# Kernel tuning notes

Measured on AMD Instinct MI355X. Metric: run time of the kernel, lower is better.

Reference implementation:

```python
import jax, jax.numpy as jnp
import numpy as np

B, T = 4096, 35          # batch rallies, max_ball_round
DSE = 227                # state_embed_dim = (37-2) + 64 + 64 + 64
C = 64                   # context_dim
H = 1024                 # hidden_dim
G5 = 25                  # GMM_num * 5
S = 12                   # shot_num
SE_NOCTX = DSE - C       # 163, state_embedding features before prior_z concat


def setup_inputs() -> dict:
    key = jax.random.key(0)
    ks = jax.random.split(key, 24)
    def r(i, shape, s=0.05):
        return (jax.random.normal(ks[i], shape, jnp.float32) * s)
    return {
        "state_embedding": r(0, (B, T, SE_NOCTX), 1.0),
        "prior_z": r(1, (B, C), 1.0),
        # state_ref_encoder (no bias)
        "W_ref": r(2, (T * DSE, DSE), 0.01),
        # f_decoder: DSE -> H -> H -> DSE with Softplus
        "fW1": r(3, (DSE, H)), "fb1": jnp.zeros((H,), jnp.float32),
        "fW2": r(4, (H, H)),   "fb2": jnp.zeros((H,), jnp.float32),
        "fW3": r(5, (H, DSE)), "fb3": jnp.zeros((DSE,), jnp.float32),
        # g_nets: DSE independent Linear(1,DSE)->Softplus->Linear(DSE,1)->Sigmoid, stacked
        "gW1": r(6, (DSE, DSE), 0.01), "gb1": r(7, (DSE, DSE), 0.01),
        "gW2": r(8, (DSE, DSE), 0.01), "gb2": r(9, (DSE,), 0.01),
        # GMM / shot heads on f_latent (no bias)
        "W_land": r(10, (DSE, G5), 0.01),
        "W_shot": r(11, (DSE, S), 0.01),
        "W_move": r(12, (DSE, G5), 0.01),
        # context_decoder: C -> H -> H -> C with Softplus
        "cW1": r(13, (C, H)), "cb1": jnp.zeros((H,), jnp.float32),
        "cW2": r(14, (H, H)), "cb2": jnp.zeros((H,), jnp.float32),
        "cW3": r(15, (H, C)), "cb3": jnp.zeros((C,), jnp.float32),
        # context GMM / shot heads (no bias)
        "cW_land": r(16, (C, G5), 0.01),
        "cW_shot": r(17, (C, S), 0.01),
        "cW_move": r(18, (C, G5), 0.01),
    }


def reference(state_embedding, prior_z, W_ref,
              fW1, fb1, fW2, fb2, fW3, fb3,
              gW1, gb1, gW2, gb2,
              W_land, W_shot, W_move,
              cW1, cb1, cW2, cb2, cW3, cb3,
              cW_land, cW_shot, cW_move):
    sp = jax.nn.softplus
    b, t, _ = state_embedding.shape

    # context_decoder(prior_z)
    ch = sp(prior_z @ cW1 + cb1)
    ch = sp(ch @ cW2 + cb2)
    ctx = ch @ cW3 + cb3                                  # [B, C]

    # repeat prior_z along time, concat, flatten, state_ref_encoder
    prior_rep = jnp.broadcast_to(prior_z[:, None, :], (b, t, prior_z.shape[-1]))
    sre = jnp.concatenate([state_embedding, prior_rep], axis=-1)  # [B, T, DSE]
    f_input = sre.reshape(b, -1) @ W_ref                  # [B, DSE]

    # f_decoder
    fh = sp(f_input @ fW1 + fb1)
    fh = sp(fh @ fW2 + fb2)
    f_latent = fh @ fW3 + fb3                             # [B, DSE]

    # g(): DSE per-dim tiny MLPs, fully vectorized as batched einsum
    gh = sp(f_latent[:, :, None] * gW1[None, :, :] + gb1[None, :, :])  # [B, DSE, DSE]
    g_out = jax.nn.sigmoid(jnp.einsum('bdh,dh->bd', gh, gW2) + gb2)    # [B, DSE]

    # GMM / shot heads
    land = f_latent @ W_land                              # [B, 25]
    shot = jax.nn.log_softmax(f_latent @ W_shot, axis=-1) # [B, 12]
    move = f_latent @ W_move                              # [B, 25]
    c_land = ctx @ cW_land
    c_shot = jax.nn.log_softmax(ctx @ cW_shot, axis=-1)
    c_move = ctx @ cW_move

    return jnp.concatenate([land, shot, move, g_out, c_land, c_shot, c_move, ctx], axis=-1)  # [B, 415]
```

## Files before the change

### kernel.cpp

```cpp
#include <hip/hip_runtime.h>
#include <hip/hip_bf16.h>

using s8 = __attribute__((ext_vector_type(8))) short;
using f4 = __attribute__((ext_vector_type(4))) float;
using us8 = __attribute__((ext_vector_type(8))) unsigned short;

__device__ __forceinline__ void glds16(const void* g, void* l) {
    __builtin_amdgcn_global_load_lds(
        (const __attribute__((address_space(1))) void*)g,
        (__attribute__((address_space(3))) void*)l, 16, 0, 0);
}

__device__ __forceinline__ unsigned short f2b(float f) {
    union { float f; unsigned u; } v; v.f = f;
    unsigned r = v.u + 0x7fffu + ((v.u >> 16) & 1u);
    return (unsigned short)(r >> 16);
}
__device__ __forceinline__ float softplus_f(float x) {
    return fmaxf(x, 0.f) + __logf(1.f + __expf(-fabsf(x)));
}
__device__ __forceinline__ float sigmoid_f(float x) {
    return 1.f / (1.f + __expf(-x));
}
__device__ __forceinline__ float exp2_f(float x) {
    float r; asm("v_exp_f32 %0, %1" : "=v"(r) : "v"(x)); return r;
}
__device__ __forceinline__ float log2_f(float x) {
    float r; asm("v_log_f32 %0, %1" : "=v"(r) : "v"(x)); return r;
}

__device__ __forceinline__ float lse12(const float* s) {
    float m = s[0];
#pragma unroll
    for (int j = 1; j < 12; j++) m = fmaxf(m, s[j]);
    float sum = 0.f;
#pragma unroll
    for (int j = 0; j < 12; j++) sum += __expf(s[j] - m);
    return m + __logf(sum);
}

__global__ __launch_bounds__(256) void prep_all_k(
    const float* __restrict__ cW1, const float* __restrict__ cW2,
    const float* __restrict__ cW3, const float* __restrict__ fW1,
    const float* __restrict__ fW2, const float* __restrict__ fW3,
    unsigned short* __restrict__ cW1T, unsigned short* __restrict__ cW2T,
    unsigned short* __restrict__ cW3T, unsigned short* __restrict__ fW1T,
    unsigned short* __restrict__ fW2T, unsigned short* __restrict__ fW3T,
    const float* __restrict__ Wref, unsigned short* __restrict__ WcatT,
    const float* __restrict__ pz, unsigned short* __restrict__ pzb,
    const float* __restrict__ gb1, const float* __restrict__ gW2,
    float* __restrict__ b1s, float* __restrict__ w2s,
    const float* __restrict__ Wl, const float* __restrict__ Ws,
    const float* __restrict__ Wm, const float* __restrict__ cWl,
    const float* __restrict__ cWs, const float* __restrict__ cWm,
    unsigned short* __restrict__ WhcT,
    const float* __restrict__ se, unsigned short* __restrict__ Acat) {
    __shared__ float tile[32][33];
    const int b = blockIdx.x, t = threadIdx.x;
    if (b < 2752) {
        int z, r = b;
        if (r < 64) { z = 0; }
        else if (r < 1088) { z = 1; r -= 64; }
        else if (r < 1216) { z = 2; r -= 1088; }
        else if (r < 1472) { z = 3; r -= 1216; }
        else if (r < 2496) { z = 4; r -= 1472; }
        else { z = 5; r -= 2496; }
        const float* src = z == 0 ? cW1 : z == 1 ? cW2 : z == 2 ? cW3
                          : z == 3 ? fW1 : z == 4 ? fW2 : fW3;
        unsigned short* dst = z == 0 ? cW1T : z == 1 ? cW2T : z == 2 ? cW3T
                             : z == 3 ? fW1T : z == 4 ? fW2T : fW3T;
        const int K    = z == 0 ? 64 : z == 3 ? 227 : 1024;
        const int N    = z == 2 ? 64 : z == 5 ? 227 : 1024;
        const int Kpad = z == 0 ? 64 : z == 3 ? 256 : 1024;
        const int Npad = z == 2 ? 128 : z == 5 ? 256 : 1024;
        const int nbx = Npad >> 5;
        const int bx = r % nbx, by = r / nbx;
        const int n0 = bx * 32, k0 = by * 32;
        const int tx = t & 31, ty = t >> 5;
#pragma unroll
        for (int rr = 0; rr < 4; rr++) {
            int k = k0 + ty + rr * 8, n = n0 + tx;
            tile[ty + rr * 8][tx] = (k < K && n < N) ? src[(size_t)k * N + n] : 0.f;
        }
        __syncthreads();
#pragma unroll
        for (int rr = 0; rr < 4; rr++) {
            int n = n0 + ty + rr * 8, k = k0 + tx;
            dst[(size_t)n * Kpad + k] = f2b(tile[tx][ty + rr * 8]);
        }
    } else if (b < 4200) {
        const int r = b - 2752;
        const int n0 = (r & 7) * 32, k0 = (r >> 3) * 32;
        const int tx = t & 31, ty = t >> 5;
#pragma unroll
        for (int rr = 0; rr < 4; rr++) {
            int k = k0 + ty + rr * 8, n = n0 + tx;
            float v = 0.f;
            if (n < 227 && k < 5769) {
                if (k < 5705) {
                    int wrow = k + 64 * (k / 163);
                    v = Wref[(size_t)wrow * 227 + n];
                } else {
                    int j2 = k - 5705;
                    for (int tt = 0; tt < 35; tt++)
                        v += Wref[(size_t)(tt * 227 + 163 + j2) * 227 + n];
                }
            }
            tile[ty + rr * 8][tx] = v;
        }
        __syncthreads();
#pragma unroll
        for (int rr = 0; rr < 4; rr++) {
            int n = n0 + ty + rr * 8, k = k0 + tx;
            if (n < 256 && k < 5792) dst_write: ;
            if (n < 256 && k < 5792)
                WcatT[(size_t)n * 5792 + k] = f2b(tile[tx][ty + rr * 8]);
        }
    } else if (b < 5586) {
        constexpr int NCVT = 4096 * 64;
        constexpr int NGS = 227 * 227;
        constexpr int NW = 128 * 320;
        int i = (b - 4200) * 256 + t;
        if (i < NCVT) {
            pzb[i] = f2b(pz[i]);
        } else if (i < NCVT + NGS) {
            int j = i - NCVT;
            b1s[j] = gb1[j] * 1.44269504f;
            w2s[j] = gW2[j] * 0.69314718f;
        } else if (i < NCVT + NGS + NW) {
            int j = i - NCVT - NGS;
            int n = j / 320, k = j - n * 320;
            float v = 0.f;
            if (n < 62 && k < 227) {
                if (n < 25)      v = Wl[(size_t)k * 25 + n];
                else if (n < 37) v = Ws[(size_t)k * 12 + (n - 25)];
                else             v = Wm[(size_t)k * 25 + (n - 37)];
            } else if (n >= 64 && n < 126 && k >= 256) {
                const int jj = n - 64, kk = k - 256;
                if (jj < 25)      v = cWl[(size_t)kk * 25 + jj];
                else if (jj < 37) v = cWs[(size_t)kk * 12 + (jj - 25)];
                else              v = cWm[(size_t)kk * 25 + (jj - 37)];
            }
            WhcT[(size_t)n * 320 + k] = f2b(v);
        }
    } else {
        const int r = b - 5586;
        const int c = (r % 3) * 256 + t;
        const int row = r / 3;
        if (c >= 724) return;
        const int col0 = c * 8;
        us8 o;
        if (col0 + 8 <= 5705) {
            const float* s = se + (size_t)row * 5705 + col0;
#pragma unroll
            for (int j = 0; j < 8; j++) o[j] = f2b(s[j]);
        } else {
#pragma unroll
            for (int j = 0; j < 8; j++) {
                int col = col0 + j;
                float v = 0.f;
                if (col < 5705) v = se[(size_t)row * 5705 + col];
                else if (col < 5769) v = pz[(size_t)row * 64 + (col - 5705)];
                o[j] = f2b(v);
            }
        }
        *(us8*)(Acat + (size_t)row * 5792 + col0) = o;
    }
}

__global__ __launch_bounds__(256) void red_enc4(const float* __restrict__ part,
                                                unsigned short* __restrict__ finb) {
    const int t = threadIdx.x;
    const int row = blockIdx.y * 4 + (t >> 6);
    const int cw = t & 63;
    if (cw < 57) {
        const float* p = part + (size_t)row * 228 + cw * 4;
        float4 s = make_float4(0.f, 0.f, 0.f, 0.f);
#pragma unroll
        for (int z = 0; z < 6; z++) {
            float4 v = *(const float4*)(p + (size_t)z * 4096 * 228);
            s.x += v.x; s.y += v.y; s.z += v.z; s.w += v.w;
        }
        if (cw == 56) s.w = 0.f;
        ushort4 o;
        o.x = f2b(s.x); o.y = f2b(s.y); o.z = f2b(s.z); o.w = f2b(s.w);
        *(ushort4*)(finb + (size_t)row * 256 + cw * 4) = o;
    } else {
        ushort4 z4 = make_ushort4(0, 0, 0, 0);
        *(ushort4*)(finb + (size_t)row * 256 + 228 + (cw - 57) * 4) = z4;
    }
}

__global__ __launch_bounds__(256) void red_cf3_k(
    const float* __restrict__ part_c3, const float* __restrict__ cb3,
    float* __restrict__ ctxb,
    const float* __restrict__ part_f3, const float* __restrict__ fb3,
    float* __restrict__ flat) {
    const int bx = blockIdx.x, t = threadIdx.x;
    if (bx < 256) {
        int idx = bx * 256 + t;
        int row = idx >> 4, c4 = idx & 15;
        float4 s = *(const float4*)(cb3 + c4 * 4);
        const float* p = part_c3 + (size_t)row * 64 + c4 * 4;
#pragma unroll
        for (int z = 0; z < 8; z++) {
            float4 v = *(const float4*)(p + (size_t)z * 4096 * 64);
            s.x += v.x; s.y += v.y; s.z += v.z; s.w += v.w;
        }
        *(float4*)(ctxb + (size_t)row * 64 + c4 * 4) = s;
    } else {
        const int by = bx - 256;
        const int row = by * 4 + (t >> 6);
        const int cw = t & 63;
        if (cw >= 57) return;
        float b[4];
#pragma unroll
        for (int j = 0; j < 4; j++) {
            int col = cw * 4 + j;
            b[j] = (col < 227) ? fb3[col] : 0.f;
        }
        const float* p = part_f3 + (size_t)row * 228 + cw * 4;
        float4 s = make_float4(b[0], b[1], b[2], b[3]);
#pragma unroll
        for (int z = 0; z < 4; z++) {
            float4 v = *(const float4*)(p + (size_t)z * 4096 * 228);
            s.x += v.x; s.y += v.y; s.z += v.z; s.w += v.w;
        }
        if (cw == 56) s.w = 0.f;
        *(float4*)(flat + (size_t)row * 228 + cw * 4) = s;
    }
}

template <int CM, int ACT, bool OBF16>
__global__ __launch_bounds__(256) void gemm_dma(
    const unsigned short* __restrict__ A, int lda,
    const unsigned short* __restrict__ WT, int ldwt,
    const float* __restrict__ bias,
    void* __restrict__ Cptr, int ldc, int N, int K, int kchunk) {
    __shared__ __align__(16) unsigned short As[128 * 32];
    __shared__ __align__(16) unsigned short Bs[128 * 32];
    const int tid = threadIdx.x;
    const int m0 = blockIdx.y * 128, n0 = blockIdx.x * 128;
    const int kbeg = blockIdx.z * kchunk;
    const int kend = min(kbeg + kchunk, K);
    const int lane = tid & 63, w = tid >> 6;
    const int wm = w >> 1, wn = w & 1;
    const int quad = lane >> 4, l16 = lane & 15;
    const int dr = lane >> 2;
    const int dk = (lane & 3) * 8;

    f4 acc[4][4] = {};

    for (int k0 = kbeg; k0 < kend; k0 += 32) {
#pragma unroll
        for (int c = 0; c < 2; c++) {
            int rr = w * 32 + c * 16;
            glds16(A + (size_t)(m0 + rr + dr) * lda + k0 + dk, &As[rr * 32]);
            glds16(WT + (size_t)(n0 + rr + dr) * ldwt + k0 + dk, &Bs[rr * 32]);
        }
        __syncthreads();
        s8 a[4], b[4];
#pragma unroll
        for (int mi = 0; mi < 4; mi++)
            a[mi] = *(const s8*)&As[(wm * 64 + mi * 16 + l16) * 32 + quad * 8];
#pragma unroll
        for (int ni = 0; ni < 4; ni++)
            b[ni] = *(const s8*)&Bs[(wn * 64 + ni * 16 + l16) * 32 + quad * 8];
#pragma unroll
        for (int mi = 0; mi < 4; mi++)
#pragma unroll
            for (int ni = 0; ni < 4; ni++)
                acc[mi][ni] = __builtin_amdgcn_mfma_f32_16x16x32_bf16(
                    a[mi], b[ni], acc[mi][ni], 0, 0, 0);
        __syncthreads();
    }

    const size_t zoff = (CM == 2) ? (size_t)blockIdx.z * 4096 * ldc : 0;
#pragma unroll
    for (int mi = 0; mi < 4; mi++) {
        int gmb = m0 + wm * 64 + mi * 16 + quad * 4;
#pragma unroll
        for (int ni = 0; ni < 4; ni++) {
            int gn = n0 + wn * 64 + ni * 16 + l16;
            if (gn < N) {
#pragma unroll
                for (int r = 0; r < 4; r++) {
                    float v = acc[mi][ni][r];
                    size_t off = (size_t)(gmb + r) * ldc + gn;
                    if (CM == 2) {
                        ((float*)Cptr)[zoff + off] = v;
                    } else {
                        if (bias) v += bias[gn];
                        if (ACT == 1) v = softplus_f(v);
                        if (OBF16) ((unsigned short*)Cptr)[off] = f2b(v);
                        else ((float*)Cptr)[off] = v;
                    }
                }
            }
        }
    }
}

__global__ __launch_bounds__(256) void gemm_dualg(
    const unsigned short* __restrict__ A0, int lda0, int K0,
    const unsigned short* __restrict__ A1, int lda1, int K1,
    const unsigned short* __restrict__ W0, int ldw0,
    const unsigned short* __restrict__ W1, int ldw1,
    const float* __restrict__ b0, const float* __restrict__ b1,
    unsigned short* __restrict__ C0, unsigned short* __restrict__ C1) {
    __shared__ __align__(16) unsigned short As[128 * 32];
    __shared__ __align__(16) unsigned short Bs[128 * 32];
    const int z = blockIdx.z;
    const unsigned short* __restrict__ A  = z ? A1 : A0;
    const unsigned short* __restrict__ WT = z ? W1 : W0;
    const float* __restrict__ bias        = z ? b1 : b0;
    unsigned short* __restrict__ C        = z ? C1 : C0;
    const int lda = z ? lda1 : lda0;
    const int ldw = z ? ldw1 : ldw0;
    const int K   = z ? K1 : K0;
    const int tid = threadIdx.x;
    const int m0 = blockIdx.y * 128, n0 = blockIdx.x * 128;
    const int lane = tid & 63, w = tid >> 6;
    const int wm = w >> 1, wn = w & 1;
    const int quad = lane >> 4, l16 = lane & 15;
    const int dr = lane >> 2;
    const int dk = (lane & 3) * 8;

    f4 acc[4][4] = {};

    for (int k0 = 0; k0 < K; k0 += 32) {
#pragma unroll
        for (int c = 0; c < 2; c++) {
            int rr = w * 32 + c * 16;
            glds16(A + (size_t)(m0 + rr + dr) * lda + k0 + dk, &As[rr * 32]);
            glds16(WT + (size_t)(n0 + rr + dr) * ldw + k0 + dk, &Bs[rr * 32]);
        }
        __syncthreads();
        s8 a[4], b[4];
#pragma unroll
        for (int mi = 0; mi < 4; mi++)
            a[mi] = *(const s8*)&As[(wm * 64 + mi * 16 + l16) * 32 + quad * 8];
#pragma unroll
        for (int ni = 0; ni < 4; ni++)
            b[ni] = *(const s8*)&Bs[(wn * 64 + ni * 16 + l16) * 32 + quad * 8];
#pragma unroll
        for (int mi = 0; mi < 4; mi++)
#pragma unroll
            for (int ni = 0; ni < 4; ni++)
                acc[mi][ni] = __builtin_amdgcn_mfma_f32_16x16x32_bf16(
                    a[mi], b[ni], acc[mi][ni], 0, 0, 0);
        __syncthreads();
    }

#pragma unroll
    for (int mi = 0; mi < 4; mi++) {
        int gmb = m0 + wm * 64 + mi * 16 + quad * 4;
#pragma unroll
        for (int ni = 0; ni < 4; ni++) {
            int gn = n0 + wn * 64 + ni * 16 + l16;
#pragma unroll
            for (int r = 0; r < 4; r++) {
                float v = acc[mi][ni][r] + bias[gn];
                C[(size_t)(gmb + r) * 1024 + gn] = f2b(softplus_f(v));
            }
        }
    }
}

__global__ __launch_bounds__(256) void part_cf3_k(
    const unsigned short* __restrict__ h2c, const unsigned short* __restrict__ cW3T,
    const unsigned short* __restrict__ h2f, const unsigned short* __restrict__ fW3T,
    float* __restrict__ part_c3, float* __restrict__ part_f3) {
    __shared__ __align__(16) unsigned short As[128 * 32];
    __shared__ __align__(16) unsigned short Bs[128 * 32];
    const int z = blockIdx.z;
    const bool isC = (z < 8);
    if (isC && blockIdx.x != 0) return;
    const unsigned short* __restrict__ A  = isC ? h2c : h2f;
    const unsigned short* __restrict__ WT = isC ? cW3T : fW3T;
    const int N   = isC ? 64 : 227;
    const int ldc = isC ? 64 : 228;
    const int zz  = isC ? z : z - 8;
    const int kbeg = zz * (isC ? 128 : 256);
    const int kend = kbeg + (isC ? 128 : 256);
    float* __restrict__ C = (isC ? part_c3 : part_f3) + (size_t)zz * 4096 * ldc;
    const int tid = threadIdx.x;
    const int m0 = blockIdx.y * 128, n0 = blockIdx.x * 128;
    const int lane = tid & 63, w = tid >> 6;
    const int wm = w >> 1, wn = w & 1;
    const int quad = lane >> 4, l16 = lane & 15;
    const int dr = lane >> 2;
    const int dk = (lane & 3) * 8;

    f4 acc[4][4] = {};

    for (int k0 = kbeg; k0 < kend; k0 += 32) {
#pragma unroll
        for (int c = 0; c < 2; c++) {
            int rr = w * 32 + c * 16;
            glds16(A + (size_t)(m0 + rr + dr) * 1024 + k0 + dk, &As[rr * 32]);
            glds16(WT + (size_t)(n0 + rr + dr) * 1024 + k0 + dk, &Bs[rr * 32]);
        }
        __syncthreads();
        s8 a[4], b[4];
#pragma unroll
        for (int mi = 0; mi < 4; mi++)
            a[mi] = *(const s8*)&As[(wm * 64 + mi * 16 + l16) * 32 + quad * 8];
#pragma unroll
        for (int ni = 0; ni < 4; ni++)
            b[ni] = *(const s8*)&Bs[(wn * 64 + ni * 16 + l16) * 32 + quad * 8];
#pragma unroll
        for (int mi = 0; mi < 4; mi++)
#pragma unroll
            for (int ni = 0; ni < 4; ni++)
                acc[mi][ni] = __builtin_amdgcn_mfma_f32_16x16x32_bf16(
                    a[mi], b[ni], acc[mi][ni], 0, 0, 0);
        __syncthreads();
    }

#pragma unroll
    for (int mi = 0; mi < 4; mi++) {
        int gmb = m0 + wm * 64 + mi * 16 + quad * 4;
#pragma unroll
        for (int ni = 0; ni < 4; ni++) {
            int gn = n0 + wn * 64 + ni * 16 + l16;
            if (gn < N) {
#pragma unroll
                for (int r = 0; r < 4; r++)
                    C[(size_t)(gmb + r) * ldc + gn] = acc[mi][ni][r];
            }
        }
    }
}

__global__ __launch_bounds__(256) void tail_k(
    const float* __restrict__ flat,
    const float* __restrict__ gW1, const float* __restrict__ b1s,
    const float* __restrict__ w2s, const float* __restrict__ gb2,
    const float* __restrict__ ctxb, unsigned short* __restrict__ Ah,
    float* __restrict__ out) {
    __shared__ float4 wt[228];
    const int bid = blockIdx.x, t = threadIdx.x;
    if (bid < 1816) {
        const int d = bid >> 3;
        const int y = bid & 7;
        if (t < 227) {
            size_t o = (size_t)d * 227 + t;
            wt[t] = make_float4(gW1[o], b1s[o], w2s[o], 0.f);
        } else if (t == 227) {
            wt[227] = make_float4(0.f, 0.f, 0.f, 0.f);
        }
        __syncthreads();
        const int b0 = y * 512 + t;
        float x0 = flat[(size_t)b0 * 228 + d] * 1.44269504f;
        float x1 = flat[(size_t)(b0 + 256) * 228 + d] * 1.44269504f;
        const float g2 = gb2[d];
        float a0 = g2, a1 = g2;
        float4 w = wt[0];
#pragma unroll 2
        for (int h = 0; h < 227; h++) {
            float4 wn = wt[h + 1];
            float z0 = fmaf(x0, w.x, w.y);
            float z1 = fmaf(x1, w.x, w.y);
            a0 = fmaf(log2_f(1.f + exp2_f(z0)), w.z, a0);
            a1 = fmaf(log2_f(1.f + exp2_f(z1)), w.z, a1);
            w = wn;
        }
        out[(size_t)b0 * 415 + 62 + d] = sigmoid_f(a0);
        out[(size_t)(b0 + 256) * 415 + 62 + d] = sigmoid_f(a1);
    } else {
        const int row = bid - 1816;
        float v = 0.f;
        if (t < 227) v = flat[(size_t)row * 228 + t];
        Ah[(size_t)row * 320 + t] = f2b(v);
        if (t < 64) Ah[(size_t)row * 320 + 256 + t] = f2b(ctxb[(size_t)row * 64 + t]);
    }
}

__global__ __launch_bounds__(256) void gemm_heads_k(
    const unsigned short* __restrict__ Ah, const unsigned short* __restrict__ WhcT,
    const float* __restrict__ ctxb, float* __restrict__ out) {
    __shared__ __align__(16) unsigned short As[128 * 32];
    __shared__ __align__(16) unsigned short Bs[128 * 32];
    __shared__ float cT[64][129];
    const int tid = threadIdx.x;
    const int m0 = blockIdx.x * 128;
    const int lane = tid & 63, w = tid >> 6;
    const int wm = w >> 1, wn = w & 1;
    const int quad = lane >> 4, l16 = lane & 15;
    const int dr = lane >> 2;
    const int dk = (lane & 3) * 8;

    f4 acc[4][4] = {};

    for (int k0 = 0; k0 < 320; k0 += 32) {
#pragma unroll
        for (int c = 0; c < 2; c++) {
            int rr = w * 32 + c * 16;
            glds16(Ah + (size_t)(m0 + rr + dr) * 320 + k0 + dk, &As[rr * 32]);
            glds16(WhcT + (size_t)(rr + dr) * 320 + k0 + dk, &Bs[rr * 32]);
        }
        __syncthreads();
        s8 a[4], b[4];
#pragma unroll
        for (int mi = 0; mi < 4; mi++)
            a[mi] = *(const s8*)&As[(wm * 64 + mi * 16 + l16) * 32 + quad * 8];
#pragma unroll
        for (int ni = 0; ni < 4; ni++)
            b[ni] = *(const s8*)&Bs[(wn * 64 + ni * 16 + l16) * 32 + quad * 8];
#pragma unroll
        for (int mi = 0; mi < 4; mi++)
#pragma unroll
            for (int ni = 0; ni < 4; ni++)
                acc[mi][ni] = __builtin_amdgcn_mfma_f32_16x16x32_bf16(
                    a[mi], b[ni], acc[mi][ni], 0, 0, 0);
        __syncthreads();
    }

#pragma unroll
    for (int pass = 0; pass < 2; pass++) {
        if (wm == pass) {
#pragma unroll
            for (int mi = 0; mi < 4; mi++) {
                int rl = mi * 16 + quad * 4;
#pragma unroll
                for (int ni = 0; ni < 4; ni++) {
                    int cl = wn * 64 + ni * 16 + l16;
#pragma unroll
                    for (int r = 0; r < 4; r++)
                        cT[rl + r][cl] = acc[mi][ni][r];
                }
            }
        }
        __syncthreads();
        if (tid < 64) {
            const int bidx = m0 + pass * 64 + tid;
            float* ob = out + (size_t)bidx * 415;
            const float* row = cT[tid];
            float sraw[12], craw[12];
#pragma unroll
            for (int j = 0; j < 25; j++) ob[j] = row[j];
#pragma unroll
            for (int j = 0; j < 12; j++) sraw[j] = row[25 + j];
#pragma unroll
            for (int j = 0; j < 25; j++) ob[37 + j] = row[37 + j];
#pragma unroll
            for (int j = 0; j < 25; j++) ob[289 + j] = row[64 + j];
#pragma unroll
            for (int j = 0; j < 12; j++) craw[j] = row[89 + j];
#pragma unroll
            for (int j = 0; j < 25; j++) ob[326 + j] = row[101 + j];
            const float lsf = lse12(sraw), lsc = lse12(craw);
#pragma unroll
            for (int j = 0; j < 12; j++) {
                ob[25 + j] = sraw[j] - lsf;
                ob[314 + j] = craw[j] - lsc;
            }
            for (int k = 0; k < 64; k++)
                ob[351 + k] = ctxb[(size_t)bidx * 64 + k];
        }
        __syncthreads();
    }
}

__global__ __launch_bounds__(256) void transpose_w(const float* __restrict__ src,
                                                   unsigned short* __restrict__ dst,
                                                   int K, int N, int Kpad, int Npad) {
    __shared__ float tile[32][33];
    const int n0 = blockIdx.x * 32, k0 = blockIdx.y * 32;
    const int tx = threadIdx.x, ty = threadIdx.y;
#pragma unroll
    for (int r = 0; r < 4; r++) {
        int k = k0 + ty + r * 8, n = n0 + tx;
        tile[ty + r * 8][tx] = (k < K && n < N) ? src[(size_t)k * N + n] : 0.f;
    }
    __syncthreads();
#pragma unroll
    for (int r = 0; r < 4; r++) {
        int n = n0 + ty + r * 8, k = k0 + tx;
        if (n < Npad && k < Kpad) dst[(size_t)n * Kpad + k] = f2b(tile[tx][ty + r * 8]);
    }
}

__global__ __launch_bounds__(256) void wcat_t(const float* __restrict__ Wref,
                                              unsigned short* __restrict__ dst) {
    __shared__ float tile[32][33];
    const int n0 = blockIdx.x * 32, k0 = blockIdx.y * 32;
    const int tx = threadIdx.x, ty = threadIdx.y;
#pragma unroll
    for (int r = 0; r < 4; r++) {
        int k = k0 + ty + r * 8, n = n0 + tx;
        float v = 0.f;
        if (n < 227 && k < 5769) {
            if (k < 5705) {
                int wrow = k + 64 * (k / 163);
                v = Wref[(size_t)wrow * 227 + n];
            } else {
                int j2 = k - 5705;
                for (int t = 0; t < 35; t++)
                    v += Wref[(size_t)(t * 227 + 163 + j2) * 227 + n];
            }
        }
        tile[ty + r * 8][tx] = v;
    }
    __syncthreads();
#pragma unroll
    for (int r = 0; r < 4; r++) {
        int n = n0 + ty + r * 8, k = k0 + tx;
        if (n < 256 && k < 5792) dst[(size_t)n * 5792 + k] = f2b(tile[tx][ty + r * 8]);
    }
}

__global__ __launch_bounds__(256) void gscale_k(const float* __restrict__ gb1,
                                                const float* __restrict__ gW2,
                                                float* __restrict__ b1s,
                                                float* __restrict__ w2s) {
    int i = blockIdx.x * 256 + threadIdx.x;
    if (i < 227 * 227) {
        b1s[i] = gb1[i] * 1.44269504f;
        w2s[i] = gW2[i] * 0.69314718f;
    }
}

__global__ __launch_bounds__(256) void fillb_k(float* __restrict__ buf,
                                               const float* __restrict__ bias,
                                               int ld, int ncr) {
    const int row = blockIdx.y;
    const int col = blockIdx.x * 256 + threadIdx.x;
    if (col >= ld) return;
    float v = 0.f;
    if (bias && col < ncr) v = bias[col];
    buf[(size_t)row * ld + col] = v;
}

template <int AMODE, int ACT, bool ATOMIC, bool OBF16>
__global__ __launch_bounds__(256) void gemm_mfma(
    const void* __restrict__ Aptr, int lda,
    const float* __restrict__ A2ptr,
    const unsigned short* __restrict__ WT, int ldwt,
    const float* __restrict__ bias,
    void* __restrict__ Cptr, int ldc,
    int M, int N, int K, int kchunk) {
    __shared__ unsigned short As[128 * 40];
    __shared__ unsigned short Bs[128 * 40];
    const int tid = threadIdx.x;
    const int m0 = blockIdx.y * 128, n0 = blockIdx.x * 128;
    const int kbeg = blockIdx.z * kchunk;
    const int kend = min(kbeg + kchunk, K);
    const int lane = tid & 63, w = tid >> 6;
    const int wm = w >> 1, wn = w & 1;
    const int quad = lane >> 4, l16 = lane & 15;

    f4 acc[4][4] = {};
    ushort4 pa[4], pb[4];

    auto loadA = [&](int k0) {
        const bool full = (kend - k0) >= 32;
#pragma unroll
        for (int i = 0; i < 4; i++) {
            int f = tid + i * 256;
            int r = f >> 3, cc = (f & 7) * 4;
            int gm = m0 + r;
            ushort4 val;
            if (AMODE == 0) {
                const float* A = (const float*)Aptr;
                float t[4];
#pragma unroll
                for (int j = 0; j < 4; j++) {
                    int k = k0 + cc + j;
                    t[j] = (k < kend) ? A[(size_t)gm * lda + k] : 0.f;
                }
                val.x = f2b(t[0]); val.y = f2b(t[1]); val.z = f2b(t[2]); val.w = f2b(t[3]);
            } else if (AMODE == 1) {
                const unsigned short* A = (const unsigned short*)Aptr;
                if (full) {
                    val = *(const ushort4*)(A + (size_t)gm * lda + k0 + cc);
                } else {
                    unsigned short t[4];
#pragma unroll
                    for (int j = 0; j < 4; j++) {
                        int k = k0 + cc + j;
                        t[j] = (k < kend) ? A[(size_t)gm * lda + k] : (unsigned short)0;
                    }
                    val.x = t[0]; val.y = t[1]; val.z = t[2]; val.w = t[3];
                }
            } else {
                const float* se = (const float*)Aptr;
                float t[4];
#pragma unroll
                for (int j = 0; j < 4; j++) {
                    int k = k0 + cc + j;
                    float v = 0.f;
                    if (k < kend) {
                        v = (k < 5705) ? se[(size_t)gm * 5705 + k]
                                       : A2ptr[(size_t)gm * 64 + (k - 5705)];
                    }
                    t[j] = v;
                }
                val.x = f2b(t[0]); val.y = f2b(t[1]); val.z = f2b(t[2]); val.w = f2b(t[3]);
            }
            pa[i] = val;
        }
    };
    auto loadB = [&](int k0) {
        const bool full = (kend - k0) >= 32;
#pragma unroll
        for (int i = 0; i < 4; i++) {
            int f = tid + i * 256;
            int r = f >> 3, cc = (f & 7) * 4;
            int gn = n0 + r;
            ushort4 val;
            if (gn < N) {
                if (full) {
                    val = *(const ushort4*)(WT + (size_t)gn * ldwt + k0 + cc);
                } else {
                    unsigned short t[4];
#pragma unroll
                    for (int j = 0; j < 4; j++) {
                        int k = k0 + cc + j;
                        t[j] = (k < kend) ? WT[(size_t)gn * ldwt + k] : (unsigned short)0;
                    }
                    val.x = t[0]; val.y = t[1]; val.z = t[2]; val.w = t[3];
                }
            } else {
                val.x = val.y = val.z = val.w = 0;
            }
            pb[i] = val;
        }
    };

    loadA(kbeg); loadB(kbeg);
    for (int k0 = kbeg; k0 < kend; k0 += 32) {
#pragma unroll
        for (int i = 0; i < 4; i++) {
            int f = tid + i * 256;
            int r = f >> 3, cc = (f & 7) * 4;
            *(ushort4*)&As[r * 40 + cc] = pa[i];
        }
#pragma unroll
        for (int i = 0; i < 4; i++) {
            int f = tid + i * 256;
            int r = f >> 3, cc = (f & 7) * 4;
            *(ushort4*)&Bs[r * 40 + cc] = pb[i];
        }
        __syncthreads();
        if (k0 + 32 < kend) { loadA(k0 + 32); loadB(k0 + 32); }
        s8 a[4], b[4];
#pragma unroll
        for (int mi = 0; mi < 4; mi++)
            a[mi] = *(const s8*)&As[(wm * 64 + mi * 16 + l16) * 40 + quad * 8];
#pragma unroll
        for (int ni = 0; ni < 4; ni++)
            b[ni] = *(const s8*)&Bs[(wn * 64 + ni * 16 + l16) * 40 + quad * 8];
#pragma unroll
        for (int mi = 0; mi < 4; mi++)
#pragma unroll
            for (int ni = 0; ni < 4; ni++)
                acc[mi][ni] = __builtin_amdgcn_mfma_f32_16x16x32_bf16(
                    a[mi], b[ni], acc[mi][ni], 0, 0, 0);
        __syncthreads();
    }
#pragma unroll
    for (int mi = 0; mi < 4; mi++) {
        int gmb = m0 + wm * 64 + mi * 16 + quad * 4;
#pragma unroll
        for (int ni = 0; ni < 4; ni++) {
            int gn = n0 + wn * 64 + ni * 16 + l16;
            if (gn < N) {
#pragma unroll
                for (int r = 0; r < 4; r++) {
                    float v = acc[mi][ni][r];
                    size_t off = (size_t)(gmb + r) * ldc + gn;
                    if (ATOMIC) {
                        atomicAdd((float*)Cptr + off, v);
                    } else {
                        if (bias) v += bias[gn];
                        if (ACT == 1) v = softplus_f(v);
                        if (OBF16) ((unsigned short*)Cptr)[off] = f2b(v);
                        else ((float*)Cptr)[off] = v;
                    }
                }
            }
        }
    }
}

__global__ __launch_bounds__(256) void g_kernel2(
    const float* __restrict__ flat,
    const float* __restrict__ gW1, const float* __restrict__ b1s,
    const float* __restrict__ w2s, const float* __restrict__ gb2,
    float* __restrict__ out) {
    __shared__ float4 wt[228];
    const int d = blockIdx.x;
    const int t = threadIdx.x;
    if (t < 227) {
        size_t o = (size_t)d * 227 + t;
        wt[t] = make_float4(gW1[o], b1s[o], w2s[o], 0.f);
    } else if (t == 227) {
        wt[227] = make_float4(0.f, 0.f, 0.f, 0.f);
    }
    __syncthreads();
    const int b0 = blockIdx.y * 512 + t;
    float x0 = flat[(size_t)b0 * 228 + d] * 1.44269504f;
    float x1 = flat[(size_t)(b0 + 256) * 228 + d] * 1.44269504f;
    const float g2 = gb2[d];
    float a0 = g2, a1 = g2;
    float4 w = wt[0];
#pragma unroll 2
    for (int h = 0; h < 227; h++) {
        float4 wn = wt[h + 1];
        float z0 = fmaf(x0, w.x, w.y);
        float z1 = fmaf(x1, w.x, w.y);
        a0 = fmaf(log2_f(1.f + exp2_f(z0)), w.z, a0);
        a1 = fmaf(log2_f(1.f + exp2_f(z1)), w.z, a1);
        w = wn;
    }
    out[(size_t)b0 * 415 + 62 + d] = sigmoid_f(a0);
    out[(size_t)(b0 + 256) * 415 + 62 + d] = sigmoid_f(a1);
}

__global__ __launch_bounds__(256) void heads_k(
    const float* __restrict__ flat, const float* __restrict__ ctx,
    const float* __restrict__ Wl, const float* __restrict__ Wsh, const float* __restrict__ Wm,
    const float* __restrict__ cWl, const float* __restrict__ cWsh, const float* __restrict__ cWm,
    float* __restrict__ out) {
    __shared__ float fl[227];
    __shared__ float cx[64];
    __shared__ float sraw[12], craw[12];
    __shared__ float lsf, lsc;
    const int b = blockIdx.x;
    const int t = threadIdx.x;
    if (t < 227) fl[t] = flat[(size_t)b * 228 + t];
    if (t < 64) cx[t] = ctx[(size_t)b * 64 + t];
    __syncthreads();
    float* ob = out + (size_t)b * 415;

    if (t < 25) {
        float a = 0.f;
        for (int k = 0; k < 227; k++) a = fmaf(fl[k], Wl[(size_t)k * 25 + t], a);
        ob[t] = a;
    } else if (t < 37) {
        int j = t - 25;
        float a = 0.f;
        for (int k = 0; k < 227; k++) a = fmaf(fl[k], Wsh[(size_t)k * 12 + j], a);
        sraw[j] = a;
    } else if (t < 62) {
        int j = t - 37;
        float a = 0.f;
        for (int k = 0; k < 227; k++) a = fmaf(fl[k], Wm[(size_t)k * 25 + j], a);
        ob[37 + j] = a;
    } else if (t >= 64 && t < 126) {
        int j2 = t - 64;
        if (j2 < 25) {
            float a = 0.f;
            for (int k = 0; k < 64; k++) a = fmaf(cx[k], cWl[(size_t)k * 25 + j2], a);
            ob[289 + j2] = a;
        } else if (j2 < 37) {
            int j = j2 - 25;
            float a = 0.f;
            for (int k = 0; k < 64; k++) a = fmaf(cx[k], cWsh[(size_t)k * 12 + j], a);
            craw[j] = a;
        } else {
            int j = j2 - 37;
            float a = 0.f;
            for (int k = 0; k < 64; k++) a = fmaf(cx[k], cWm[(size_t)k * 25 + j], a);
            ob[326 + j] = a;
        }
    } else if (t >= 128 && t < 192) {
        ob[351 + (t - 128)] = cx[t - 128];
    }
    __syncthreads();
    if (t == 0) lsf = lse12(sraw);
    if (t == 64) lsc = lse12(craw);
    __syncthreads();
    if (t < 12) ob[25 + t] = sraw[t] - lsf;
    else if (t >= 64 && t < 76) ob[314 + (t - 64)] = craw[t - 64] - lsc;
}

extern "C" void kernel_launch(void* const* d_in, const int* in_sizes, int n_in,
                              void* d_out, int out_size, void* d_ws, size_t ws_size,
                              hipStream_t stream) {
    const float* se    = (const float*)d_in[0];
    const float* pz    = (const float*)d_in[1];
    const float* Wref  = (const float*)d_in[2];
    const float* fW1   = (const float*)d_in[3];
    const float* fb1   = (const float*)d_in[4];
    const float* fW2   = (const float*)d_in[5];
    const float* fb2   = (const float*)d_in[6];
    const float* fW3   = (const float*)d_in[7];
    const float* fb3   = (const float*)d_in[8];
    const float* gW1   = (const float*)d_in[9];
    const float* gb1   = (const float*)d_in[10];
    const float* gW2   = (const float*)d_in[11];
    const float* gb2   = (const float*)d_in[12];
    const float* Wland = (const float*)d_in[13];
    const float* Wshot = (const float*)d_in[14];
    const float* Wmove = (const float*)d_in[15];
    const float* cW1   = (const float*)d_in[16];
    const float* cb1   = (const float*)d_in[17];
    const float* cW2   = (const float*)d_in[18];
    const float* cb2   = (const float*)d_in[19];
    const float* cW3   = (const float*)d_in[20];
    const float* cb3   = (const float*)d_in[21];
    const float* cWl   = (const float*)d_in[22];
    const float* cWs   = (const float*)d_in[23];
    const float* cWm   = (const float*)d_in[24];
    float* out = (float*)d_out;
    const int M = 4096;

    char* p = (char*)d_ws;
    auto alloc = [&](size_t bytes) {
        char* r = p;
        p += (bytes + 255) & ~(size_t)255;
        return r;
    };
    unsigned short* WcatT = (unsigned short*)alloc((size_t)256 * 5792 * 2);
    unsigned short* cW1T  = (unsigned short*)alloc((size_t)1024 * 64 * 2);
    unsigned short* cW2T  = (unsigned short*)alloc((size_t)1024 * 1024 * 2);
    unsigned short* cW3T  = (unsigned short*)alloc((size_t)128 * 1024 * 2);
    unsigned short* fW1T  = (unsigned short*)alloc((size_t)1024 * 256 * 2);
    unsigned short* fW2T  = (unsigned short*)alloc((size_t)1024 * 1024 * 2);
    unsigned short* fW3T  = (unsigned short*)alloc((size_t)256 * 1024 * 2);
    float* fin  = (float*)alloc((size_t)M * 228 * 4);
    float* flat = (float*)alloc((size_t)M * 228 * 4);
    float* ctxb = (float*)alloc((size_t)M * 64 * 4);
    unsigned short* h2b  = (unsigned short*)alloc((size_t)M * 1024 * 2);
    unsigned short* h1fb = (unsigned short*)alloc((size_t)M * 1024 * 2);
    float* b1s = (float*)alloc((size_t)227 * 227 * 4);
    float* w2s = (float*)alloc((size_t)227 * 227 * 4);

    size_t base_used = (size_t)(p - (char*)d_ws);
    size_t full_extra = (size_t)M * 64 * 2
                      + (size_t)M * 256 * 2
                      + (size_t)M * 5792 * 2
                      + (size_t)128 * 320 * 2 + 1024;
    const bool full = (base_used + full_extra + 65536) <= ws_size;

    if (full) {
        unsigned short* pzb  = (unsigned short*)alloc((size_t)M * 64 * 2);
        unsigned short* finb = (unsigned short*)alloc((size_t)M * 256 * 2);
        char* region = alloc((size_t)M * 5792 * 2);
        unsigned short* WhcT = (unsigned short*)alloc((size_t)128 * 320 * 2);
        unsigned short* Acat = (unsigned short*)region;
        float* part_enc = fin;
        unsigned short* h2fb   = (unsigned short*)region;
        float* part_c3         = (float*)(region + (size_t)8 * 1024 * 1024);
        unsigned short* h1f    = (unsigned short*)(region + (size_t)16 * 1024 * 1024);
        float* part_f3         = (float*)(region + (size_t)24 * 1024 * 1024);
        unsigned short* Ah     = (unsigned short*)(region + (size_t)41 * 1024 * 1024);
        unsigned short* h1c = h1fb;
        unsigned short* h2c = h2b;

        prep_all_k<<<dim3(17874), 256, 0, stream>>>(
            cW1, cW2, cW3, fW1, fW2, fW3, cW1T, cW2T, cW3T, fW1T, fW2T, fW3T,
            Wref, WcatT, pz, pzb, gb1, gW2, b1s, w2s,
            Wland, Wshot, Wmove, cWl, cWs, cWm, WhcT, se, Acat);

        gemm_dma<2, 0, false><<<dim3(2, 32, 6), 256, 0, stream>>>(
            Acat, 5792, WcatT, 5792, nullptr, part_enc, 228, 227, 5792, 992);
        red_enc4<<<dim3(1, 1024), 256, 0, stream>>>(part_enc, finb);

        gemm_dualg<<<dim3(8, 32, 2), 256, 0, stream>>>(
            pzb, 64, 64, finb, 256, 256, cW1T, 64, fW1T, 256, cb1, fb1, h1c, h1f);
        gemm_dualg<<<dim3(8, 32, 2), 256, 0, stream>>>(
            h1c, 1024, 1024, h1f, 1024, 1024, cW2T, 1024, fW2T, 1024, cb2, fb2, h2c, h2fb);

        part_cf3_k<<<dim3(2, 32, 12), 256, 0, stream>>>(
            h2c, cW3T, h2fb, fW3T, part_c3, part_f3);
        red_cf3_k<<<dim3(1280), 256, 0, stream>>>(
            part_c3, cb3, ctxb, part_f3, fb3, flat);

        tail_k<<<dim3(5912), 256, 0, stream>>>(
            flat, gW1, b1s, w2s, gb2, ctxb, Ah, out);

        gemm_heads_k<<<dim3(32), 256, 0, stream>>>(Ah, WhcT, ctxb, out);
    } else {
        const dim3 tb(32, 8);
        transpose_w<<<dim3(32, 2),  tb, 0, stream>>>(cW1, cW1T, 64, 1024, 64, 1024);
        transpose_w<<<dim3(32, 32), tb, 0, stream>>>(cW2, cW2T, 1024, 1024, 1024, 1024);
        transpose_w<<<dim3(4, 32),  tb, 0, stream>>>(cW3, cW3T, 1024, 64, 1024, 128);
        transpose_w<<<dim3(32, 8),  tb, 0, stream>>>(fW1, fW1T, 227, 1024, 256, 1024);
        transpose_w<<<dim3(32, 32), tb, 0, stream>>>(fW2, fW2T, 1024, 1024, 1024, 1024);
        transpose_w<<<dim3(8, 32),  tb, 0, stream>>>(fW3, fW3T, 1024, 227, 1024, 256);
        wcat_t<<<dim3(8, 181), tb, 0, stream>>>(Wref, WcatT);
        gscale_k<<<dim3(202), 256, 0, stream>>>(gb1, gW2, b1s, w2s);
        fillb_k<<<dim3(1, M), 256, 0, stream>>>(fin, nullptr, 228, 0);
        fillb_k<<<dim3(1, M), 256, 0, stream>>>(flat, fb3, 228, 227);
        fillb_k<<<dim3(1, M), 256, 0, stream>>>(ctxb, cb3, 64, 64);
        unsigned short* h1 = h1fb;
        gemm_mfma<0, 1, false, true><<<dim3(8, 32, 1), 256, 0, stream>>>(
            pz, 64, nullptr, cW1T, 64, cb1, h1, 1024, M, 1024, 64, 64);
        gemm_mfma<1, 1, false, true><<<dim3(8, 32, 1), 256, 0, stream>>>(
            h1, 1024, nullptr, cW2T, 1024, cb2, h2b, 1024, M, 1024, 1024, 1024);
        gemm_mfma<1, 0, true, false><<<dim3(1, 32, 8), 256, 0, stream>>>(
            h2b, 1024, nullptr, cW3T, 1024, nullptr, ctxb, 64, M, 64, 1024, 128);
        gemm_mfma<2, 0, true, false><<<dim3(2, 32, 8), 256, 0, stream>>>(
            se, 5705, pz, WcatT, 5792, nullptr, fin, 228, M, 227, 5769, 736);
        gemm_mfma<0, 1, false, true><<<dim3(8, 32, 1), 256, 0, stream>>>(
            fin, 228, nullptr, fW1T, 256, fb1, h1, 1024, M, 1024, 227, 227);
        gemm_mfma<1, 1, false, true><<<dim3(8, 32, 1), 256, 0, stream>>>(
            h1, 1024, nullptr, fW2T, 1024, fb2, h2b, 1024, M, 1024, 1024, 1024);
        gemm_mfma<1, 0, true, false><<<dim3(2, 32, 8), 256, 0, stream>>>(
            h2b, 1024, nullptr, fW3T, 1024, nullptr, flat, 228, M, 227, 1024, 128);
        heads_k<<<dim3(4096), 256, 0, stream>>>(flat, ctxb, Wland, Wshot, Wmove,
                                                cWl, cWs, cWm, out);
        g_kernel2<<<dim3(227, 8), 256, 0, stream>>>(flat, gW1, b1s, w2s, gb2, out);
    }
}
```

Baseline: 379.1 us.

## Fuse fp32-to-bf16 activation conversion into encoder split-K GEMM

Measured after the change: 433.9 us. 14.5% more time.

```diff
diff --git a/kernel.cpp b/kernel.cpp
--- a/kernel.cpp
+++ b/kernel.cpp
@@ -53,8 +53,7 @@
     const float* __restrict__ Wl, const float* __restrict__ Ws,
     const float* __restrict__ Wm, const float* __restrict__ cWl,
     const float* __restrict__ cWs, const float* __restrict__ cWm,
-    unsigned short* __restrict__ WhcT,
-    const float* __restrict__ se, unsigned short* __restrict__ Acat) {
+    unsigned short* __restrict__ WhcT) {
     __shared__ float tile[32][33];
     const int b = blockIdx.x, t = threadIdx.x;
     if (b < 2752) {
@@ -112,11 +111,10 @@
 #pragma unroll
         for (int rr = 0; rr < 4; rr++) {
             int n = n0 + ty + rr * 8, k = k0 + tx;
-            if (n < 256 && k < 5792) dst_write: ;
             if (n < 256 && k < 5792)
                 WcatT[(size_t)n * 5792 + k] = f2b(tile[tx][ty + rr * 8]);
         }
-    } else if (b < 5586) {
+    } else {
         constexpr int NCVT = 4096 * 64;
         constexpr int NGS = 227 * 227;
         constexpr int NW = 128 * 320;
@@ -143,28 +141,120 @@
             }
             WhcT[(size_t)n * 320 + k] = f2b(v);
         }
-    } else {
-        const int r = b - 5586;
-        const int c = (r % 3) * 256 + t;
-        const int row = r / 3;
-        if (c >= 724) return;
-        const int col0 = c * 8;
-        us8 o;
-        if (col0 + 8 <= 5705) {
-            const float* s = se + (size_t)row * 5705 + col0;
-#pragma unroll
-            for (int j = 0; j < 8; j++) o[j] = f2b(s[j]);
-        } else {
-#pragma unroll
-            for (int j = 0; j < 8; j++) {
-                int col = col0 + j;
+    }
+}
+
+__global__ __launch_bounds__(256) void gemm_encp(
+    const float* __restrict__ se, const float* __restrict__ pz,
+    const unsigned short* __restrict__ WT,
+    float* __restrict__ part) {
+    __shared__ unsigned short As[128 * 40];
+    __shared__ unsigned short Bs[128 * 40];
+    const int tid = threadIdx.x;
+    const int m0 = blockIdx.y * 128, n0 = blockIdx.x * 128;
+    const int kbeg = blockIdx.z * 992;
+    const int kend = min(kbeg + 992, 5769);
+    const int lane = tid & 63, w = tid >> 6;
+    const int wm = w >> 1, wn = w & 1;
+    const int quad = lane >> 4, l16 = lane & 15;
+
+    f4 acc[4][4] = {};
+    ushort4 pa[4], pb[4];
+
+    auto loadA = [&](int k0) {
+#pragma unroll
+        for (int i = 0; i < 4; i++) {
+            int f = tid + i * 256;
+            int r = f >> 3, cc = (f & 7) * 4;
+            int gm = m0 + r;
+            float tv[4];
+#pragma unroll
+            for (int j = 0; j < 4; j++) {
+                int k = k0 + cc + j;
                 float v = 0.f;
-                if (col < 5705) v = se[(size_t)row * 5705 + col];
-                else if (col < 5769) v = pz[(size_t)row * 64 + (col - 5705)];
-                o[j] = f2b(v);
-            }
-        }
-        *(us8*)(Acat + (size_t)row * 5792 + col0) = o;
+                if (k < kend) {
+                    v = (k < 5705) ? se[(size_t)gm * 5705 + k]
+                                   : pz[(size_t)gm * 64 + (k - 5705)];
+                }
+                tv[j] = v;
+            }
+            ushort4 val;
+            val.x = f2b(tv[0]); val.y = f2b(tv[1]); val.z = f2b(tv[2]); val.w = f2b(tv[3]);
+            pa[i] = val;
+        }
+    };
+    auto loadB = [&](int k0) {
+        const bool full = (kend - k0) >= 32;
+#pragma unroll
+        for (int i = 0; i < 4; i++) {
+            int f = tid + i * 256;
+            int r = f >> 3, cc = (f & 7) * 4;
+            int gn = n0 + r;
+            ushort4 val;
+            if (gn < 227) {
+                if (full) {
+                    val = *(const ushort4*)(WT + (size_t)gn * 5792 + k0 + cc);
+                } else {
+                    unsigned short tv[4];
+#pragma unroll
+                    for (int j = 0; j < 4; j++) {
+                        int k = k0 + cc + j;
+                        tv[j] = (k < kend) ? WT[(size_t)gn * 5792 + k] : (unsigned short)0;
+                    }
+                    val.x = tv[0]; val.y = tv[1]; val.z = tv[2]; val.w = tv[3];
+                }
+            } else {
+                val.x = val.y = val.z = val.w = 0;
+            }
+            pb[i] = val;
+        }
+    };
+
+    loadA(kbeg); loadB(kbeg);
+    for (int k0 = kbeg; k0 < kend; k0 += 32) {
+#pragma unroll
+        for (int i = 0; i < 4; i++) {
+            int f = tid + i * 256;
+            int r = f >> 3, cc = (f & 7) * 4;
+            *(ushort4*)&As[r * 40 + cc] = pa[i];
+        }
+#pragma unroll
+        for (int i = 0; i < 4; i++) {
+            int f = tid + i * 256;
+            int r = f >> 3, cc = (f & 7) * 4;
+            *(ushort4*)&Bs[r * 40 + cc] = pb[i];
+        }
+        __syncthreads();
+        if (k0 + 32 < kend) { loadA(k0 + 32); loadB(k0 + 32); }
+        s8 a[4], b[4];
+#pragma unroll
+        for (int mi = 0; mi < 4; mi++)
+            a[mi] = *(const s8*)&As[(wm * 64 + mi * 16 + l16) * 40 + quad * 8];
+#pragma unroll
+        for (int ni = 0; ni < 4; ni++)
+            b[ni] = *(const s8*)&Bs[(wn * 64 + ni * 16 + l16) * 40 + quad * 8];
+#pragma unroll
+        for (int mi = 0; mi < 4; mi++)
+#pragma unroll
+            for (int ni = 0; ni < 4; ni++)
+                acc[mi][ni] = __builtin_amdgcn_mfma_f32_16x16x32_bf16(
+                    a[mi], b[ni], acc[mi][ni], 0, 0, 0);
+        __syncthreads();
+    }
+
+    float* C = part + (size_t)blockIdx.z * 4096 * 228;
+#pragma unroll
+    for (int mi = 0; mi < 4; mi++) {
+        int gmb = m0 + wm * 64 + mi * 16 + quad * 4;
+#pragma unroll
+        for (int ni = 0; ni < 4; ni++) {
+            int gn = n0 + wn * 64 + ni * 16 + l16;
+            if (gn < 227) {
+#pragma unroll
+                for (int r = 0; r < 4; r++)
+                    C[(size_t)(gmb + r) * 228 + gn] = acc[mi][ni][r];
+            }
+        }
     }
 }
 
@@ -228,76 +318,6 @@
         }
         if (cw == 56) s.w = 0.f;
         *(float4*)(flat + (size_t)row * 228 + cw * 4) = s;
-    }
-}
-
-template <int CM, int ACT, bool OBF16>
-__global__ __launch_bounds__(256) void gemm_dma(
-    const unsigned short* __restrict__ A, int lda,
-    const unsigned short* __restrict__ WT, int ldwt,
-    const float* __restrict__ bias,
-    void* __restrict__ Cptr, int ldc, int N, int K, int kchunk) {
-    __shared__ __align__(16) unsigned short As[128 * 32];
-    __shared__ __align__(16) unsigned short Bs[128 * 32];
-    const int tid = threadIdx.x;
-    const int m0 = blockIdx.y * 128, n0 = blockIdx.x * 128;
-    const int kbeg = blockIdx.z * kchunk;
-    const int kend = min(kbeg + kchunk, K);
-    const int lane = tid & 63, w = tid >> 6;
-    const int wm = w >> 1, wn = w & 1;
-    const int quad = lane >> 4, l16 = lane & 15;
-    const int dr = lane >> 2;
-    const int dk = (lane & 3) * 8;
-
-    f4 acc[4][4] = {};
-
-    for (int k0 = kbeg; k0 < kend; k0 += 32) {
-#pragma unroll
-        for (int c = 0; c < 2; c++) {
-            int rr = w * 32 + c * 16;
-            glds16(A + (size_t)(m0 + rr + dr) * lda + k0 + dk, &As[rr * 32]);
-            glds16(WT + (size_t)(n0 + rr + dr) * ldwt + k0 + dk, &Bs[rr * 32]);
-        }
-        __syncthreads();
-        s8 a[4], b[4];
-#pragma unroll
-        for (int mi = 0; mi < 4; mi++)
-            a[mi] = *(const s8*)&As[(wm * 64 + mi * 16 + l16) * 32 + quad * 8];
-#pragma unroll
-        for (int ni = 0; ni < 4; ni++)
-            b[ni] = *(const s8*)&Bs[(wn * 64 + ni * 16 + l16) * 32 + quad * 8];
-#pragma unroll
-        for (int mi = 0; mi < 4; mi++)
-#pragma unroll
-            for (int ni = 0; ni < 4; ni++)
-                acc[mi][ni] = __builtin_amdgcn_mfma_f32_16x16x32_bf16(
-                    a[mi], b[ni], acc[mi][ni], 0, 0, 0);
-        __syncthreads();
-    }
-
-    const size_t zoff = (CM == 2) ? (size_t)blockIdx.z * 4096 * ldc : 0;
-#pragma unroll
-    for (int mi = 0; mi < 4; mi++) {
-        int gmb = m0 + wm * 64 + mi * 16 + quad * 4;
-#pragma unroll
-        for (int ni = 0; ni < 4; ni++) {
-            int gn = n0 + wn * 64 + ni * 16 + l16;
-            if (gn < N) {
-#pragma unroll
-                for (int r = 0; r < 4; r++) {
-                    float v = acc[mi][ni][r];
-                    size_t off = (size_t)(gmb + r) * ldc + gn;
-                    if (CM == 2) {
-                        ((float*)Cptr)[zoff + off] = v;
-                    } else {
-                        if (bias) v += bias[gn];
-                        if (ACT == 1) v = softplus_f(v);
-                        if (OBF16) ((unsigned short*)Cptr)[off] = f2b(v);
-                        else ((float*)Cptr)[off] = v;
-                    }
-                }
-            }
-        }
     }
 }
 
@@ -941,7 +961,6 @@
         unsigned short* finb = (unsigned short*)alloc((size_t)M * 256 * 2);
         char* region = alloc((size_t)M * 5792 * 2);
         unsigned short* WhcT = (unsigned short*)alloc((size_t)128 * 320 * 2);
-        unsigned short* Acat = (unsigned short*)region;
         float* part_enc = fin;
         unsigned short* h2fb   = (unsigned short*)region;
         float* part_c3         = (float*)(region + (size_t)8 * 1024 * 1024);
@@ -951,13 +970,12 @@
         unsigned short* h1c = h1fb;
         unsigned short* h2c = h2b;
 
-        prep_all_k<<<dim3(17874), 256, 0, stream>>>(
+        prep_all_k<<<dim3(5586), 256, 0, stream>>>(
             cW1, cW2, cW3, fW1, fW2, fW3, cW1T, cW2T, cW3T, fW1T, fW2T, fW3T,
             Wref, WcatT, pz, pzb, gb1, gW2, b1s, w2s,
-            Wland, Wshot, Wmove, cWl, cWs, cWm, WhcT, se, Acat);
-
-        gemm_dma<2, 0, false><<<dim3(2, 32, 6), 256, 0, stream>>>(
-            Acat, 5792, WcatT, 5792, nullptr, part_enc, 228, 227, 5792, 992);
+            Wland, Wshot, Wmove, cWl, cWs, cWm, WhcT);
+
+        gemm_encp<<<dim3(2, 32, 6), 256, 0, stream>>>(se, pz, WcatT, part_enc);
         red_enc4<<<dim3(1, 1024), 256, 0, stream>>>(part_enc, finb);
 
         gemm_dualg<<<dim3(8, 32, 2), 256, 0, stream>>>(
```
